# Performance work log

Hardware: AMD Instinct MI355X
Metric: run time of the kernel (lower is better)

The kernel has to match this reference:

```python
import jax, jax.numpy as jnp
import numpy as np

B, H, W = 64, 16, 16
DIMS = [2048, 1024, 512, 256, 128, 1]


def _target_fc(x, w, b):
    # x: [B, in, H, W]; w: [B, out, in, 1, 1]; b: [B, out]
    # Equivalent to grouped 1x1 conv2d with groups=B (per-sample FC over channels).
    y = jnp.einsum('boi,bihw->bohw', w[:, :, :, 0, 0], x)
    return y + b[:, :, None, None]


def setup_inputs() -> dict:
    key = jax.random.key(0)
    ks = jax.random.split(key, 11)
    inp = {'x': jax.random.normal(ks[0], (B, DIMS[0], H, W), dtype=jnp.float32)}
    for i in range(5):
        din, dout = DIMS[i], DIMS[i + 1]
        scale = 1.0 / np.sqrt(din)
        inp[f'w{i+1}'] = jax.random.normal(ks[1 + 2 * i], (B, dout, din, 1, 1), dtype=jnp.float32) * scale
        inp[f'b{i+1}'] = jax.random.normal(ks[2 + 2 * i], (B, dout), dtype=jnp.float32) * scale
    return inp


def reference(x, w1, b1, w2, b2, w3, b3, w4, b4, w5, b5):
    q = jax.nn.sigmoid(_target_fc(x, w1, b1))
    q = jax.nn.sigmoid(_target_fc(q, w2, b2))
    q = jax.nn.sigmoid(_target_fc(q, w3, b3))
    q = jax.nn.sigmoid(_target_fc(q, w4, b4))
    q = _target_fc(q, w5, b5)
    return jnp.squeeze(q)  # [B, H, W]
```

## Files before the change

### kernel.cpp

```cpp
#include <hip/hip_runtime.h>
#include <hip/hip_bf16.h>
#include <cstdint>

#define DEVINL __device__ __forceinline__

typedef __attribute__((ext_vector_type(8))) short bf16x8;
typedef __attribute__((ext_vector_type(4))) float f32x4;

DEVINL unsigned short f2bf(float f) {
    union { float f; unsigned u; } v; v.f = f;
    unsigned r = v.u + 0x7fffu + ((v.u >> 16) & 1u);
    return (unsigned short)(r >> 16);
}
DEVINL float bf2f(unsigned short h) {
    union { unsigned u; float f; } v; v.u = ((unsigned)h) << 16;
    return v.f;
}

constexpr int BN = 256, BK = 32;
constexpr int PITCH = 40;
constexpr int NSP = 256;

__global__ __launch_bounds__(256)
void xpose(const float* __restrict__ x, unsigned short* __restrict__ xT)
{
    __shared__ float sh[64][65];
    const int b   = blockIdx.y;
    const int kt  = blockIdx.x & 31;
    const int ntb = blockIdx.x >> 5;
    const int k0 = kt * 64, n0 = ntb * 64;

    const int r = threadIdx.x >> 4;
    const int c = (threadIdx.x & 15) * 4;

    const float* xb = x + ((size_t)b * 2048 + k0) * 256 + n0;
#pragma unroll
    for (int i = 0; i < 4; ++i) {
        float4 v = *(const float4*)(xb + (size_t)(r + 16 * i) * 256 + c);
        sh[r + 16 * i][c + 0] = v.x;
        sh[r + 16 * i][c + 1] = v.y;
        sh[r + 16 * i][c + 2] = v.z;
        sh[r + 16 * i][c + 3] = v.w;
    }
    __syncthreads();
#pragma unroll
    for (int i = 0; i < 4; ++i) {
        const int rr = r + 16 * i;
        ushort4 o;
        o.x = f2bf(sh[c + 0][rr]);
        o.y = f2bf(sh[c + 1][rr]);
        o.z = f2bf(sh[c + 2][rr]);
        o.w = f2bf(sh[c + 3][rr]);
        *(ushort4*)(xT + ((size_t)b * NSP + n0 + rr) * 2048 + k0 + c) = o;
    }
}

template<int BM, int WM, int WN>
__global__ __launch_bounds__(512, 2)
void fc_gemm(const float* __restrict__ Wt, const float* __restrict__ bias,
             const unsigned short* __restrict__ X, unsigned short* __restrict__ Yt,
             int M, int K)
{
    constexpr int TM = BM / WM;
    constexpr int TN = BN / WN;
    constexpr int AM = TM / 16;
    constexpr int AN = TN / 16;
    constexpr int AI = BM / 64;

    const int b  = blockIdx.y;
    const int m0 = blockIdx.x * BM;

    __shared__ __align__(16) unsigned short sA[2][BM * PITCH];
    __shared__ __align__(16) unsigned short sB[2][BN * PITCH];

    const int tid  = threadIdx.x;
    const int lane = tid & 63;
    const int wid  = tid >> 6;
    const int wm   = (wid / WN) * TM;
    const int wn   = (wid % WN) * TN;
    const int fr   = lane & 15;
    const int fo   = (lane >> 4) * 8;

    const int am = (AI == 2) ? (tid >> 2) : (tid >> 3);
    const int ac = (AI == 2) ? (tid & 3) * 4 : (tid & 7) * 4;
    const float* Wb = Wt + (size_t)b * M * K + (size_t)m0 * K;

    const int bn = tid >> 1;
    const int bc = (tid & 1) * 16;
    const unsigned short* Xb = X + (size_t)b * NSP * K;

    float4 aR[AI];
    uint4  bR[2];

    auto loadA = [&](int k0) {
#pragma unroll
        for (int i = 0; i < AI; ++i)
            aR[i] = *(const float4*)(Wb + (size_t)am * K + k0 + ac + i * 16);
    };
    auto loadB = [&](int k0) {
#pragma unroll
        for (int i = 0; i < 2; ++i)
            bR[i] = *(const uint4*)(Xb + (size_t)bn * K + k0 + bc + i * 8);
    };
    auto storeA = [&](int buf) {
#pragma unroll
        for (int i = 0; i < AI; ++i) {
            ushort4 p;
            p.x = f2bf(aR[i].x); p.y = f2bf(aR[i].y);
            p.z = f2bf(aR[i].z); p.w = f2bf(aR[i].w);
            *(ushort4*)&sA[buf][am * PITCH + ac + i * 16] = p;
        }
    };
    auto storeB = [&](int buf) {
#pragma unroll
        for (int i = 0; i < 2; ++i)
            *(uint4*)&sB[buf][bn * PITCH + bc + i * 8] = bR[i];
    };

    f32x4 acc[AM][AN] = {};

    loadA(0); loadB(0);
    storeA(0); storeB(0);
    __syncthreads();

    const int NT = K / BK;
    int cur = 0;
#pragma unroll 1
    for (int t = 0; t < NT; ++t) {
        if (t + 1 < NT) { loadA((t + 1) * BK); loadB((t + 1) * BK); }

        bf16x8 af[AM], bfr[AN];
#pragma unroll
        for (int i = 0; i < AM; ++i)
            af[i] = *(const bf16x8*)&sA[cur][(wm + i * 16 + fr) * PITCH + fo];
#pragma unroll
        for (int i = 0; i < AN; ++i)
            bfr[i] = *(const bf16x8*)&sB[cur][(wn + i * 16 + fr) * PITCH + fo];
#pragma unroll
        for (int mi = 0; mi < AM; ++mi)
#pragma unroll
            for (int ni = 0; ni < AN; ++ni)
                acc[mi][ni] = __builtin_amdgcn_mfma_f32_16x16x32_bf16(af[mi], bfr[ni], acc[mi][ni], 0, 0, 0);

        if (t + 1 < NT) { storeA(cur ^ 1); storeB(cur ^ 1); }
        __syncthreads();
        cur ^= 1;
    }

    const bool SIG = (M != 1);
    (void)SIG;
#pragma unroll
    for (int mi = 0; mi < AM; ++mi) {
#pragma unroll
        for (int ni = 0; ni < AN; ++ni) {
            const int n  = wn + ni * 16 + fr;
            const int mb = m0 + wm + mi * 16 + (lane >> 4) * 4;
            f32x4 v = acc[mi][ni];
            ushort4 o;
#pragma unroll
            for (int q = 0; q < 4; ++q) {
                float yv = v[q] + bias[(size_t)b * M + mb + q];
                yv = 1.0f / (1.0f + __expf(-yv));
                ((unsigned short*)&o)[q] = f2bf(yv);
            }
            *(ushort4*)&Yt[((size_t)b * NSP + n) * M + mb] = o;
        }
    }
}

__global__ void fc_final(const unsigned short* __restrict__ A4,
                         const float* __restrict__ W5,
                         const float* __restrict__ B5,
                         float* __restrict__ out)
{
    const int b = blockIdx.x;
    const int t = threadIdx.x;
    const unsigned short* row = A4 + ((size_t)b * NSP + t) * 128;
    const float* w = W5 + (size_t)b * 128;
    float acc = B5[b];
#pragma unroll
    for (int k = 0; k < 128; k += 8) {
        uint4 v = *(const uint4*)(row + k);
        acc += bf2f((unsigned short)(v.x & 0xffff)) * w[k+0];
        acc += bf2f((unsigned short)(v.x >> 16))    * w[k+1];
        acc += bf2f((unsigned short)(v.y & 0xffff)) * w[k+2];
        acc += bf2f((unsigned short)(v.y >> 16))    * w[k+3];
        acc += bf2f((unsigned short)(v.z & 0xffff)) * w[k+4];
        acc += bf2f((unsigned short)(v.z >> 16))    * w[k+5];
        acc += bf2f((unsigned short)(v.w & 0xffff)) * w[k+6];
        acc += bf2f((unsigned short)(v.w >> 16))    * w[k+7];
    }
    out[b * NSP + t] = acc;
}

extern "C" void kernel_launch(void* const* d_in, const int* in_sizes, int n_in,
                              void* d_out, int out_size, void* d_ws, size_t ws_size,
                              hipStream_t stream)
{
    const float* x  = (const float*)d_in[0];
    const float* w1 = (const float*)d_in[1];
    const float* b1 = (const float*)d_in[2];
    const float* w2 = (const float*)d_in[3];
    const float* b2 = (const float*)d_in[4];
    const float* w3 = (const float*)d_in[5];
    const float* b3 = (const float*)d_in[6];
    const float* w4 = (const float*)d_in[7];
    const float* b4 = (const float*)d_in[8];
    const float* w5 = (const float*)d_in[9];
    const float* b5 = (const float*)d_in[10];

    unsigned short* ws0 = (unsigned short*)d_ws;

    const size_t XT   = (size_t)64 * 256 * 2048;
    unsigned short* xT   = ws0;
    unsigned short* act1 = ws0 + XT;
    unsigned short* act2 = ws0;
    unsigned short* act3 = ws0 + (size_t)64 * 256 * 512;
    unsigned short* act4 = ws0 + (size_t)64 * 256 * (512+256);

    xpose<<<dim3(128, 64), dim3(256), 0, stream>>>(x, xT);
    fc_gemm<128, 2, 4><<<dim3(8, 64), dim3(512), 0, stream>>>(w1, b1, xT,   act1, 1024, 2048);
    fc_gemm<128, 2, 4><<<dim3(4, 64), dim3(512), 0, stream>>>(w2, b2, act1, act2,  512, 1024);
    fc_gemm< 64, 1, 8><<<dim3(4, 64), dim3(512), 0, stream>>>(w3, b3, act2, act3,  256,  512);
    fc_gemm< 64, 1, 8><<<dim3(2, 64), dim3(512), 0, stream>>>(w4, b4, act3, act4,  128,  256);
    fc_final<<<dim3(64), dim3(256), 0, stream>>>(act4, w5, b5, (float*)d_out);
}
```

Before: 376.8 us.

## Stage GEMM epilogue through shared memory for coalesced stores, swap grid axes

```diff
diff --git a/kernel.cpp b/kernel.cpp
--- a/kernel.cpp
+++ b/kernel.cpp
@@ -56,7 +56,7 @@
 }
 
 template<int BM, int WM, int WN>
-__global__ __launch_bounds__(512, 2)
+__global__ __launch_bounds__(512, 4)
 void fc_gemm(const float* __restrict__ Wt, const float* __restrict__ bias,
              const unsigned short* __restrict__ X, unsigned short* __restrict__ Yt,
              int M, int K)
@@ -66,12 +66,14 @@
     constexpr int AM = TM / 16;
     constexpr int AN = TN / 16;
     constexpr int AI = BM / 64;
-
-    const int b  = blockIdx.y;
-    const int m0 = blockIdx.x * BM;
-
-    __shared__ __align__(16) unsigned short sA[2][BM * PITCH];
-    __shared__ __align__(16) unsigned short sB[2][BN * PITCH];
+    constexpr int EPP = BM + 8;
+
+    const int b  = blockIdx.x;
+    const int m0 = blockIdx.y * BM;
+
+    __shared__ __align__(16) unsigned short smem[(2 * BM + 2 * BN) * PITCH];
+    unsigned short* sA0 = smem;
+    unsigned short* sB0 = smem + 2 * BM * PITCH;
 
     const int tid  = threadIdx.x;
     const int lane = tid & 63;
@@ -103,18 +105,20 @@
             bR[i] = *(const uint4*)(Xb + (size_t)bn * K + k0 + bc + i * 8);
     };
     auto storeA = [&](int buf) {
+        unsigned short* s = sA0 + buf * BM * PITCH;
 #pragma unroll
         for (int i = 0; i < AI; ++i) {
             ushort4 p;
             p.x = f2bf(aR[i].x); p.y = f2bf(aR[i].y);
             p.z = f2bf(aR[i].z); p.w = f2bf(aR[i].w);
-            *(ushort4*)&sA[buf][am * PITCH + ac + i * 16] = p;
+            *(ushort4*)&s[am * PITCH + ac + i * 16] = p;
         }
     };
     auto storeB = [&](int buf) {
+        unsigned short* s = sB0 + buf * BN * PITCH;
 #pragma unroll
         for (int i = 0; i < 2; ++i)
-            *(uint4*)&sB[buf][bn * PITCH + bc + i * 8] = bR[i];
+            *(uint4*)&s[bn * PITCH + bc + i * 8] = bR[i];
     };
 
     f32x4 acc[AM][AN] = {};
@@ -129,13 +133,15 @@
     for (int t = 0; t < NT; ++t) {
         if (t + 1 < NT) { loadA((t + 1) * BK); loadB((t + 1) * BK); }
 
+        const unsigned short* a = sA0 + cur * BM * PITCH;
+        const unsigned short* bb = sB0 + cur * BN * PITCH;
         bf16x8 af[AM], bfr[AN];
 #pragma unroll
         for (int i = 0; i < AM; ++i)
-            af[i] = *(const bf16x8*)&sA[cur][(wm + i * 16 + fr) * PITCH + fo];
+            af[i] = *(const bf16x8*)&a[(wm + i * 16 + fr) * PITCH + fo];
 #pragma unroll
         for (int i = 0; i < AN; ++i)
-            bfr[i] = *(const bf16x8*)&sB[cur][(wn + i * 16 + fr) * PITCH + fo];
+            bfr[i] = *(const bf16x8*)&bb[(wn + i * 16 + fr) * PITCH + fo];
 #pragma unroll
         for (int mi = 0; mi < AM; ++mi)
 #pragma unroll
@@ -147,24 +153,40 @@
         cur ^= 1;
     }
 
-    const bool SIG = (M != 1);
-    (void)SIG;
-#pragma unroll
-    for (int mi = 0; mi < AM; ++mi) {
-#pragma unroll
-        for (int ni = 0; ni < AN; ++ni) {
-            const int n  = wn + ni * 16 + fr;
-            const int mb = m0 + wm + mi * 16 + (lane >> 4) * 4;
-            f32x4 v = acc[mi][ni];
-            ushort4 o;
-#pragma unroll
-            for (int q = 0; q < 4; ++q) {
-                float yv = v[q] + bias[(size_t)b * M + mb + q];
-                yv = 1.0f / (1.0f + __expf(-yv));
-                ((unsigned short*)&o)[q] = f2bf(yv);
+    const int hi4 = (lane >> 4) * 4;
+#pragma unroll 1
+    for (int ph = 0; ph < 2; ++ph) {
+        if ((wn >> 7) == ph) {
+#pragma unroll
+            for (int mi = 0; mi < AM; ++mi) {
+#pragma unroll
+                for (int ni = 0; ni < AN; ++ni) {
+                    const int r  = (wn & 127) + ni * 16 + fr;
+                    const int mb = wm + mi * 16 + hi4;
+                    f32x4 v = acc[mi][ni];
+                    ushort4 o;
+#pragma unroll
+                    for (int q = 0; q < 4; ++q) {
+                        float yv = v[q] + bias[(size_t)b * M + m0 + mb + q];
+                        yv = 1.0f / (1.0f + __expf(-yv));
+                        ((unsigned short*)&o)[q] = f2bf(yv);
+                    }
+                    *(ushort4*)&smem[r * EPP + mb] = o;
+                }
             }
-            *(ushort4*)&Yt[((size_t)b * NSP + n) * M + mb] = o;
         }
+        __syncthreads();
+        constexpr int TPR = BM / 8;
+        constexpr int RPI = 512 / TPR;
+        const int r = tid / TPR;
+        const int c = (tid % TPR) * 8;
+#pragma unroll
+        for (int it = 0; it < 128 / RPI; ++it) {
+            const int rr = r + it * RPI;
+            uint4 v = *(const uint4*)&smem[rr * EPP + c];
+            *(uint4*)&Yt[((size_t)b * NSP + ph * 128 + rr) * M + m0 + c] = v;
+        }
+        __syncthreads();
     }
 }
 
@@ -211,17 +233,17 @@
 
     unsigned short* ws0 = (unsigned short*)d_ws;
 
-    const size_t XT   = (size_t)64 * 256 * 2048;
+    const size_t XT = (size_t)64 * 256 * 2048;
     unsigned short* xT   = ws0;
     unsigned short* act1 = ws0 + XT;
     unsigned short* act2 = ws0;
     unsigned short* act3 = ws0 + (size_t)64 * 256 * 512;
-    unsigned short* act4 = ws0 + (size_t)64 * 256 * (512+256);
+    unsigned short* act4 = ws0 + (size_t)64 * 256 * (512 + 256);
 
     xpose<<<dim3(128, 64), dim3(256), 0, stream>>>(x, xT);
-    fc_gemm<128, 2, 4><<<dim3(8, 64), dim3(512), 0, stream>>>(w1, b1, xT,   act1, 1024, 2048);
-    fc_gemm<128, 2, 4><<<dim3(4, 64), dim3(512), 0, stream>>>(w2, b2, act1, act2,  512, 1024);
-    fc_gemm< 64, 1, 8><<<dim3(4, 64), dim3(512), 0, stream>>>(w3, b3, act2, act3,  256,  512);
-    fc_gemm< 64, 1, 8><<<dim3(2, 64), dim3(512), 0, stream>>>(w4, b4, act3, act4,  128,  256);
+    fc_gemm<128, 2, 4><<<dim3(64, 8), dim3(512), 0, stream>>>(w1, b1, xT,   act1, 1024, 2048);
+    fc_gemm<128, 2, 4><<<dim3(64, 4), dim3(512), 0, stream>>>(w2, b2, act1, act2,  512, 1024);
+    fc_gemm< 64, 1, 8><<<dim3(64, 4), dim3(512), 0, stream>>>(w3, b3, act2, act3,  256,  512);
+    fc_gemm< 64, 1, 8><<<dim3(64, 2), dim3(512), 0, stream>>>(w4, b4, act3, act4,  128,  256);
     fc_final<<<dim3(64), dim3(256), 0, stream>>>(act4, w5, b5, (float*)d_out);
 }
```

New measurement: 377.2 us. About the same (+0.1%).
